# Kernel tuning notes

Measured on AMD Instinct MI355X. Metric: run time of the kernel, lower is better.

The kernel has to match this reference:

```python
import jax, jax.numpy as jnp
import numpy as np

B, R, D, H, C = 256, 100, 6168, 128, 100  # batch, replicas, in_dim, hidden, classes


def setup_inputs() -> dict:
    key = jax.random.key(0)
    k1, k2, k3, k4, k5, k6 = jax.random.split(key, 6)
    # binary input features (texas dataset is binary; original casts to bool)
    x = jax.random.randint(k1, (B, D), 0, 2).astype(jnp.int32)
    # Bernoulli(0.5) flip mask, one per replica per feature
    noise = jax.random.randint(k2, (B, R, D), 0, 2).astype(jnp.int32)
    s1 = 1.0 / np.sqrt(D)
    W1 = jax.random.uniform(k3, (D, H), minval=-s1, maxval=s1, dtype=jnp.float32)
    b1 = jax.random.uniform(k4, (H,), minval=-s1, maxval=s1, dtype=jnp.float32)
    s2 = 1.0 / np.sqrt(H)
    W2 = jax.random.uniform(k5, (H, C), minval=-s2, maxval=s2, dtype=jnp.float32)
    b2 = jax.random.uniform(k6, (C,), minval=-s2, maxval=s2, dtype=jnp.float32)
    return {"x": x, "noise": noise, "W1": W1, "b1": b1, "W2": W2, "b2": b2}


def reference(x, noise, W1, b1, W2, b2):
    # np.invert(x, where=noise) on booleans == flip bit where noise==1
    xb = x[:, None, :]                                   # [B,1,D]
    x_noisy = jnp.where(noise == 1, 1 - xb, xb).astype(W1.dtype)  # [B,R,D]
    h = jnp.tanh(jnp.einsum('brd,dh->brh', x_noisy, W1) + b1)      # [B,R,H]
    logits = jnp.einsum('brh,hc->brc', h, W2) + b2                 # [B,R,C]
    return logits.mean(axis=1)                                     # [B,C]
```

## Files before the change

kernel.cpp:

```cpp
#include <hip/hip_runtime.h>
#include <hip/hip_bf16.h>

#define NB 256
#define NR 100
#define NRH 50
#define ND 6168
#define DP 6272
#define NH 128
#define NC 100
#define NSUP (DP / 128)
#define W1T_BYTES ((size_t)NH * DP * 2)

typedef __attribute__((ext_vector_type(8))) __bf16 bf16x8;
typedef __attribute__((ext_vector_type(4))) float f32x4;
typedef __attribute__((ext_vector_type(4))) int i32x4;
typedef __attribute__((ext_vector_type(4))) unsigned int u32x4;
typedef unsigned int u32;

typedef const __attribute__((address_space(1))) u32* gas_ptr;
typedef __attribute__((address_space(3))) u32* las_ptr;

__device__ __forceinline__ void gload16(const void* g, void* l) {
  __builtin_amdgcn_global_load_lds((gas_ptr)g, (las_ptr)l, 16, 0, 0);
}

#define VBAR(N) do { \
  __builtin_amdgcn_sched_barrier(0); \
  asm volatile("s_waitcnt vmcnt(" #N ")"); \
  __builtin_amdgcn_sched_barrier(0); \
  __builtin_amdgcn_s_barrier(); \
  __builtin_amdgcn_sched_barrier(0); \
} while (0)

__global__ void prep_w1t(const float* __restrict__ W1, __hip_bfloat16* __restrict__ W1T) {
  __shared__ float tile[32][NH + 1];
  const int d0 = blockIdx.x * 32;
  const int t = threadIdx.x;
#pragma unroll
  for (int p = 0; p < 16; ++p) {
    int idx = p * 256 + t;
    int dd = idx >> 7;
    int h  = idx & 127;
    int d  = d0 + dd;
    tile[dd][h] = (d < ND) ? W1[d * NH + h] : 0.f;
  }
  __syncthreads();
#pragma unroll
  for (int p = 0; p < 16; ++p) {
    int idx = p * 256 + t;
    int h  = idx >> 5;
    int dd = idx & 31;
    W1T[h * DP + d0 + dd] = __float2bfloat16(tile[dd][h]);
  }
}

__launch_bounds__(256, 2)
__global__ void fused_main(const int* __restrict__ x,
                           const int* __restrict__ noise,
                           const __hip_bfloat16* __restrict__ W1T,
                           const float* __restrict__ b1,
                           float* __restrict__ partials) {
  __shared__ __align__(16) char lds[78080];
  u32* xpair = (u32*)lds;
  char* const A0 = lds + 12544;
  char* const A1 = A0 + 32768;

  const int tid  = threadIdx.x;
  const int lane = tid & 63;
  const int w    = tid >> 6;
  const int lq   = lane >> 4;
  const int lm   = lane & 15;
  const int bid  = blockIdx.x;
  const int b    = bid >> 1;
  const int half = bid & 1;

  const size_t nbase = (size_t)b * NR * ND;

  f32x4 acc[4][2] = {};

  struct Bregs { bf16x8 f[8]; };
  Bregs B0r, B1r;

  auto STAGE = [&](int s, char* dst) {
#pragma unroll
    for (int i = 0; i < 8; ++i) {
      const int call = w * 8 + i;
      const int row  = call * 2 + (lane >> 5);
      const int gr   = half * NRH + ((row < NRH) ? row : (NRH - 1));
      const int slot = lane & 31;
      const int slotp = slot ^ (row & 7);
      int kint = s * 128 + slotp * 4;
      kint = (kint + 4 <= ND) ? kint : 0;
      gload16(noise + nbase + (size_t)gr * ND + kint, dst + call * 1024);
    }
  };

  auto BLOAD = [&](int s, Bregs& Br) {
#pragma unroll
    for (int kt = 0; kt < 4; ++kt)
#pragma unroll
      for (int nf = 0; nf < 2; ++nf)
        Br.f[kt * 2 + nf] = *(const bf16x8*)(W1T + (size_t)(w * 32 + nf * 16 + lm) * DP
                                             + s * 128 + kt * 32 + lq * 8);
  };

  auto COMPUTE = [&](int s, const char* Ab, const Bregs& Br) {
#pragma unroll
    for (int kt = 0; kt < 4; ++kt) {
      u32x4 xp = *(const u32x4*)(xpair + s * 64 + kt * 16 + lq * 4);
#pragma unroll
      for (int mf = 0; mf < 4; ++mf) {
        const int row = mf * 16 + lm;
        const int s0  = kt * 8 + lq * 2;
        const char* base = Ab + row * 512;
        i32x4 v0 = *(const i32x4*)(base + ((s0    ) ^ (row & 7)) * 16);
        i32x4 v1 = *(const i32x4*)(base + ((s0 + 1) ^ (row & 7)) * 16);
        u32 pk0 = (((u32)v0[0] | ((u32)v0[1] << 16)) ^ xp[0]) * 0x3F80u;
        u32 pk1 = (((u32)v0[2] | ((u32)v0[3] << 16)) ^ xp[1]) * 0x3F80u;
        u32 pk2 = (((u32)v1[0] | ((u32)v1[1] << 16)) ^ xp[2]) * 0x3F80u;
        u32 pk3 = (((u32)v1[2] | ((u32)v1[3] << 16)) ^ xp[3]) * 0x3F80u;
        u32x4 pkv = {pk0, pk1, pk2, pk3};
        bf16x8 af = *(bf16x8*)&pkv;
        acc[mf][0] = __builtin_amdgcn_mfma_f32_16x16x32_bf16(af, Br.f[kt * 2 + 0], acc[mf][0], 0, 0, 0);
        acc[mf][1] = __builtin_amdgcn_mfma_f32_16x16x32_bf16(af, Br.f[kt * 2 + 1], acc[mf][1], 0, 0, 0);
      }
    }
  };

  STAGE(0, A0);
  BLOAD(0, B0r);
  {
    const int* xb = x + b * ND;
    for (int i = tid; i < DP / 2; i += 256) {
      unsigned p = 0;
      if (2 * i + 1 < ND) {
        int2 v = *(const int2*)(xb + 2 * i);
        p = ((unsigned)v.x & 1u) | (((unsigned)v.y & 1u) << 16);
      }
      xpair[i] = p;
    }
  }
  __syncthreads();

  for (int s = 0; s < NSUP - 1; s += 2) {
    VBAR(8);
    STAGE(s + 1, A1);
    BLOAD(s + 1, B1r);
    COMPUTE(s, A0, B0r);

    VBAR(8);
    if (s + 2 < NSUP) { STAGE(s + 2, A0); BLOAD(s + 2, B0r); }
    COMPUTE(s + 1, A1, B1r);
  }
  VBAR(8);
  COMPUTE(NSUP - 1, A0, B0r);

#pragma unroll
  for (int nf = 0; nf < 2; ++nf) {
    int hcol = w * 32 + nf * 16 + lm;
    float bb = b1[hcol];
    float ssum = 0.f;
#pragma unroll
    for (int mf = 0; mf < 4; ++mf) {
#pragma unroll
      for (int rg = 0; rg < 4; ++rg) {
        int m = mf * 16 + lq * 4 + rg;
        float tv = tanhf(acc[mf][nf][rg] + bb);
        ssum += (m < NRH) ? tv : 0.f;
      }
    }
    ssum += __shfl_xor(ssum, 16, 64);
    ssum += __shfl_xor(ssum, 32, 64);
    if (lq == 0) partials[(size_t)bid * NH + hcol] = ssum;
  }
}

__global__ void combine(const float* __restrict__ partials,
                        const float* __restrict__ W2,
                        const float* __restrict__ b2,
                        float* __restrict__ out) {
  __shared__ float hbar[NH];
  const int b = blockIdx.x;
  const int t = threadIdx.x;
  if (t < NH)
    hbar[t] = (partials[(size_t)(2 * b) * NH + t] + partials[(size_t)(2 * b + 1) * NH + t]) * (1.0f / NR);
  __syncthreads();
  if (t < NC) {
    float s = b2[t];
#pragma unroll 8
    for (int h = 0; h < NH; ++h) s += hbar[h] * W2[h * NC + t];
    out[b * NC + t] = s;
  }
}

extern "C" void kernel_launch(void* const* d_in, const int* in_sizes, int n_in,
                              void* d_out, int out_size, void* d_ws, size_t ws_size,
                              hipStream_t stream) {
  (void)in_sizes; (void)n_in; (void)out_size; (void)ws_size;
  const int* x     = (const int*)d_in[0];
  const int* noise = (const int*)d_in[1];
  const float* W1  = (const float*)d_in[2];
  const float* b1  = (const float*)d_in[3];
  const float* W2  = (const float*)d_in[4];
  const float* b2  = (const float*)d_in[5];
  float* out = (float*)d_out;

  __hip_bfloat16* W1T = (__hip_bfloat16*)d_ws;
  float* partials = (float*)((char*)d_ws + W1T_BYTES);

  prep_w1t<<<DP / 32, 256, 0, stream>>>(W1, W1T);
  fused_main<<<2 * NB, 256, 0, stream>>>(x, noise, W1T, b1, partials);
  combine<<<NB, 128, 0, stream>>>(partials, W2, b2, out);
}
```

Baseline: 211.9 us.

## Use one 512-thread block per batch with 4-deep noise pipeline and fused combine

Each batch element is now handled by a single 512-thread block (2x4 wave grid over replicas x hidden) instead of two 256-thread blocks. Noise staging moves to 64-column segments with a four-buffer ring and three stages in flight, and per-lane source pointers are precomputed. The final W2 projection is folded into the main kernel, so the separate combine launch and the partials round-trip disappear. The block needs about 140KB of LDS, which limits occupancy to one block per CU, and it pads replicas 100 to 128, so some MFMA work is wasted.

```diff
diff --git a/kernel.cpp b/kernel.cpp
--- a/kernel.cpp
+++ b/kernel.cpp
@@ -3,12 +3,13 @@
 
 #define NB 256
 #define NR 100
-#define NRH 50
 #define ND 6168
 #define DP 6272
 #define NH 128
 #define NC 100
-#define NSUP (DP / 128)
+#define NSEG 98
+#define ABUF 32768
+#define ROWB 24672
 #define W1T_BYTES ((size_t)NH * DP * 2)
 
 typedef __attribute__((ext_vector_type(8))) __bf16 bf16x8;
@@ -24,13 +25,9 @@
   __builtin_amdgcn_global_load_lds((gas_ptr)g, (las_ptr)l, 16, 0, 0);
 }
 
-#define VBAR(N) do { \
-  __builtin_amdgcn_sched_barrier(0); \
-  asm volatile("s_waitcnt vmcnt(" #N ")"); \
-  __builtin_amdgcn_sched_barrier(0); \
-  __builtin_amdgcn_s_barrier(); \
-  __builtin_amdgcn_sched_barrier(0); \
-} while (0)
+#define SB() __builtin_amdgcn_sched_barrier(0)
+#define VBAR16() do { SB(); asm volatile("s_waitcnt vmcnt(16)"); SB(); \
+  asm volatile("s_waitcnt lgkmcnt(0)"); SB(); __builtin_amdgcn_s_barrier(); SB(); } while (0)
 
 __global__ void prep_w1t(const float* __restrict__ W1, __hip_bfloat16* __restrict__ W1T) {
   __shared__ float tile[32][NH + 1];
@@ -54,72 +51,83 @@
   }
 }
 
-__launch_bounds__(256, 2)
+__launch_bounds__(512, 2)
 __global__ void fused_main(const int* __restrict__ x,
                            const int* __restrict__ noise,
                            const __hip_bfloat16* __restrict__ W1T,
                            const float* __restrict__ b1,
-                           float* __restrict__ partials) {
-  __shared__ __align__(16) char lds[78080];
+                           const float* __restrict__ W2,
+                           const float* __restrict__ b2,
+                           float* __restrict__ out) {
+  __shared__ __align__(16) char lds[12544 + 4 * ABUF];
   u32* xpair = (u32*)lds;
-  char* const A0 = lds + 12544;
-  char* const A1 = A0 + 32768;
+  char* const Ab = lds + 12544;
 
   const int tid  = threadIdx.x;
   const int lane = tid & 63;
   const int w    = tid >> 6;
+  const int wm   = w >> 2;
+  const int wn   = w & 3;
   const int lq   = lane >> 4;
   const int lm   = lane & 15;
-  const int bid  = blockIdx.x;
-  const int b    = bid >> 1;
-  const int half = bid & 1;
-
-  const size_t nbase = (size_t)b * NR * ND;
+  const int b    = blockIdx.x;
+
+  const char* nsrc[4];
+  u32 offmax[4];
+  int dofs[4];
+  {
+    const size_t nb = (size_t)b * NR * ND;
+#pragma unroll
+    for (int i = 0; i < 4; ++i) {
+      int c   = w * 4 + i;
+      int row = c * 4 + (lane >> 4);
+      int gr  = (row < NR) ? row : (NR - 1);
+      int sg  = (lane & 15) ^ (row & 7);
+      nsrc[i]   = (const char*)(noise + nb + (size_t)gr * ND) + sg * 16;
+      offmax[i] = (u32)(ROWB - 16 - sg * 16);
+      dofs[i]   = c * 1024;
+    }
+  }
+  const __hip_bfloat16* wsrc0 = W1T + (size_t)(wn * 32 + lm) * DP + lq * 8;
+  const __hip_bfloat16* wsrc1 = W1T + (size_t)(wn * 32 + 16 + lm) * DP + lq * 8;
 
   f32x4 acc[4][2] = {};
-
-  struct Bregs { bf16x8 f[8]; };
-  Bregs B0r, B1r;
-
-  auto STAGE = [&](int s, char* dst) {
-#pragma unroll
-    for (int i = 0; i < 8; ++i) {
-      const int call = w * 8 + i;
-      const int row  = call * 2 + (lane >> 5);
-      const int gr   = half * NRH + ((row < NRH) ? row : (NRH - 1));
-      const int slot = lane & 31;
-      const int slotp = slot ^ (row & 7);
-      int kint = s * 128 + slotp * 4;
-      kint = (kint + 4 <= ND) ? kint : 0;
-      gload16(noise + nbase + (size_t)gr * ND + kint, dst + call * 1024);
+  struct Bregs { bf16x8 f[4]; };
+  Bregs Bcur, Bnxt;
+
+  auto STAGE = [&](int ss, int bufidx) {
+    char* dstb = Ab + bufidx * ABUF;
+    const u32 off = (u32)(ss * 256);
+#pragma unroll
+    for (int i = 0; i < 4; ++i) {
+      u32 o = (off > offmax[i]) ? offmax[i] : off;
+      gload16(nsrc[i] + o, dstb + dofs[i]);
     }
   };
 
   auto BLOAD = [&](int s, Bregs& Br) {
 #pragma unroll
-    for (int kt = 0; kt < 4; ++kt)
-#pragma unroll
-      for (int nf = 0; nf < 2; ++nf)
-        Br.f[kt * 2 + nf] = *(const bf16x8*)(W1T + (size_t)(w * 32 + nf * 16 + lm) * DP
-                                             + s * 128 + kt * 32 + lq * 8);
+    for (int kt = 0; kt < 2; ++kt) {
+      Br.f[kt * 2 + 0] = *(const bf16x8*)(wsrc0 + s * 64 + kt * 32);
+      Br.f[kt * 2 + 1] = *(const bf16x8*)(wsrc1 + s * 64 + kt * 32);
+    }
   };
 
-  auto COMPUTE = [&](int s, const char* Ab, const Bregs& Br) {
-#pragma unroll
-    for (int kt = 0; kt < 4; ++kt) {
-      u32x4 xp = *(const u32x4*)(xpair + s * 64 + kt * 16 + lq * 4);
+  auto COMPUTE = [&](int s, const char* A, const Bregs& Br) {
+#pragma unroll
+    for (int kt = 0; kt < 2; ++kt) {
+      u32x4 xp = *(const u32x4*)(xpair + s * 32 + kt * 16 + lq * 4);
 #pragma unroll
       for (int mf = 0; mf < 4; ++mf) {
-        const int row = mf * 16 + lm;
-        const int s0  = kt * 8 + lq * 2;
-        const char* base = Ab + row * 512;
-        i32x4 v0 = *(const i32x4*)(base + ((s0    ) ^ (row & 7)) * 16);
-        i32x4 v1 = *(const i32x4*)(base + ((s0 + 1) ^ (row & 7)) * 16);
-        u32 pk0 = (((u32)v0[0] | ((u32)v0[1] << 16)) ^ xp[0]) * 0x3F80u;
-        u32 pk1 = (((u32)v0[2] | ((u32)v0[3] << 16)) ^ xp[1]) * 0x3F80u;
-        u32 pk2 = (((u32)v1[0] | ((u32)v1[1] << 16)) ^ xp[2]) * 0x3F80u;
-        u32 pk3 = (((u32)v1[2] | ((u32)v1[3] << 16)) ^ xp[3]) * 0x3F80u;
-        u32x4 pkv = {pk0, pk1, pk2, pk3};
+        const int row  = wm * 64 + mf * 16 + lm;
+        const int off0 = row * 256 + (((kt * 8 + lq * 2) ^ (row & 7)) * 16);
+        i32x4 v0 = *(const i32x4*)(A + off0);
+        i32x4 v1 = *(const i32x4*)(A + (off0 ^ 16));
+        u32 q0 = (((u32)v0[0] | ((u32)v0[1] << 16)) ^ xp[0]) * 0x3F80u;
+        u32 q1 = (((u32)v0[2] | ((u32)v0[3] << 16)) ^ xp[1]) * 0x3F80u;
+        u32 q2 = (((u32)v1[0] | ((u32)v1[1] << 16)) ^ xp[2]) * 0x3F80u;
+        u32 q3 = (((u32)v1[2] | ((u32)v1[3] << 16)) ^ xp[3]) * 0x3F80u;
+        u32x4 pkv = {q0, q1, q2, q3};
         bf16x8 af = *(bf16x8*)&pkv;
         acc[mf][0] = __builtin_amdgcn_mfma_f32_16x16x32_bf16(af, Br.f[kt * 2 + 0], acc[mf][0], 0, 0, 0);
         acc[mf][1] = __builtin_amdgcn_mfma_f32_16x16x32_bf16(af, Br.f[kt * 2 + 1], acc[mf][1], 0, 0, 0);
@@ -127,69 +135,76 @@
     }
   };
 
-  STAGE(0, A0);
-  BLOAD(0, B0r);
+  STAGE(0, 0);
+  STAGE(1, 1);
+  STAGE(2, 2);
+  BLOAD(0, Bcur);
   {
     const int* xb = x + b * ND;
-    for (int i = tid; i < DP / 2; i += 256) {
-      unsigned p = 0;
+    for (int i = tid; i < DP / 2; i += 512) {
+      u32 p = 0;
       if (2 * i + 1 < ND) {
         int2 v = *(const int2*)(xb + 2 * i);
-        p = ((unsigned)v.x & 1u) | (((unsigned)v.y & 1u) << 16);
+        p = ((u32)v.x & 1u) | (((u32)v.y & 1u) << 16);
       }
       xpair[i] = p;
     }
   }
   __syncthreads();
 
-  for (int s = 0; s < NSUP - 1; s += 2) {
-    VBAR(8);
-    STAGE(s + 1, A1);
-    BLOAD(s + 1, B1r);
-    COMPUTE(s, A0, B0r);
-
-    VBAR(8);
-    if (s + 2 < NSUP) { STAGE(s + 2, A0); BLOAD(s + 2, B0r); }
-    COMPUTE(s + 1, A1, B1r);
-  }
-  VBAR(8);
-  COMPUTE(NSUP - 1, A0, B0r);
-
+#pragma unroll 1
+  for (int s = 0; s < NSEG; s += 2) {
+    {
+      VBAR16();
+      int sn = (s + 1 < NSEG) ? (s + 1) : (NSEG - 1);
+      BLOAD(sn, Bnxt);
+      SB();
+      int sc = (s + 3 < NSEG) ? (s + 3) : (NSEG - 1);
+      STAGE(sc, (s + 3) & 3);
+      SB();
+      COMPUTE(s, Ab + (s & 3) * ABUF, Bcur);
+    }
+    {
+      VBAR16();
+      int sn = (s + 2 < NSEG) ? (s + 2) : (NSEG - 1);
+      BLOAD(sn, Bcur);
+      SB();
+      int sc = (s + 4 < NSEG) ? (s + 4) : (NSEG - 1);
+      STAGE(sc, (s + 4) & 3);
+      SB();
+      COMPUTE(s + 1, Ab + ((s + 1) & 3) * ABUF, Bnxt);
+    }
+  }
+
+  __syncthreads();
+  float* hpart = (float*)lds;
+  float* hbar  = (float*)(lds + 1024);
 #pragma unroll
   for (int nf = 0; nf < 2; ++nf) {
-    int hcol = w * 32 + nf * 16 + lm;
+    int hcol = wn * 32 + nf * 16 + lm;
     float bb = b1[hcol];
     float ssum = 0.f;
 #pragma unroll
     for (int mf = 0; mf < 4; ++mf) {
 #pragma unroll
       for (int rg = 0; rg < 4; ++rg) {
-        int m = mf * 16 + lq * 4 + rg;
+        int m = wm * 64 + mf * 16 + lq * 4 + rg;
         float tv = tanhf(acc[mf][nf][rg] + bb);
-        ssum += (m < NRH) ? tv : 0.f;
+        ssum += (m < NR) ? tv : 0.f;
       }
     }
     ssum += __shfl_xor(ssum, 16, 64);
     ssum += __shfl_xor(ssum, 32, 64);
-    if (lq == 0) partials[(size_t)bid * NH + hcol] = ssum;
-  }
-}
-
-__global__ void combine(const float* __restrict__ partials,
-                        const float* __restrict__ W2,
-                        const float* __restrict__ b2,
-                        float* __restrict__ out) {
-  __shared__ float hbar[NH];
-  const int b = blockIdx.x;
-  const int t = threadIdx.x;
-  if (t < NH)
-    hbar[t] = (partials[(size_t)(2 * b) * NH + t] + partials[(size_t)(2 * b + 1) * NH + t]) * (1.0f / NR);
-  __syncthreads();
-  if (t < NC) {
-    float s = b2[t];
+    if (lq == 0) hpart[wm * 128 + hcol] = ssum;
+  }
+  __syncthreads();
+  if (tid < NH) hbar[tid] = (hpart[tid] + hpart[128 + tid]) * (1.0f / NR);
+  __syncthreads();
+  if (tid < NC) {
+    float sacc = b2[tid];
 #pragma unroll 8
-    for (int h = 0; h < NH; ++h) s += hbar[h] * W2[h * NC + t];
-    out[b * NC + t] = s;
+    for (int h = 0; h < NH; ++h) sacc += hbar[h] * W2[h * NC + tid];
+    out[b * NC + tid] = sacc;
   }
 }
 
@@ -206,9 +221,7 @@
   float* out = (float*)d_out;
 
   __hip_bfloat16* W1T = (__hip_bfloat16*)d_ws;
-  float* partials = (float*)((char*)d_ws + W1T_BYTES);
 
   prep_w1t<<<DP / 32, 256, 0, stream>>>(W1, W1T);
-  fused_main<<<2 * NB, 256, 0, stream>>>(x, noise, W1T, b1, partials);
-  combine<<<NB, 128, 0, stream>>>(partials, W2, b2, out);
-}
+  fused_main<<<NB, 512, 0, stream>>>(x, noise, W1T, b1, W2, b2, out);
+}
```

New measurement: 211.7 us, median of 2. Within noise of the previous version (-0.1%).
